# Optimization experiments

Hardware: AMD Instinct MI355X
Metric: run time of the kernel (lower is better)

Reference implementation:

```python
import jax, jax.numpy as jnp
import numpy as np

SEGMENT_LENGTHS = [2048, 4096, 8192]
DILATION_RATES = [1, 2, 4]
RING_SIZE = 4


def _head_groups(h, g):
    base, rem = divmod(h, g)
    return [base + (1 if i < rem else 0) for i in range(g)]


def _dilation_pattern(n, seg, r, group_idx):
    # Per-segment dilated index pattern of total length n (index_select target).
    s = min(seg, n)
    off = group_idx % r
    base = (off + np.arange(0, s, r)) % s          # stride-r indices within segment
    pat_seg = np.tile(base, r)[:s]                  # repeat to fill segment length
    nseg = n // s
    pat = (pat_seg[None, :] + np.arange(nseg)[:, None] * s).reshape(-1)
    return pat


def _apply_dilation(x):
    # x: (b, n, h, d). Gather along sequence per head group.
    b, n, h, d = x.shape
    groups = _head_groups(h, len(SEGMENT_LENGTHS))
    outs, hs = [], 0
    for i, (seg, r, g) in enumerate(zip(SEGMENT_LENGTHS, DILATION_RATES, groups)):
        if g == 0:
            continue
        pat = jnp.asarray(_dilation_pattern(n, seg, r, i))
        outs.append(x[:, pat, hs:hs + g, :])
        hs += g
    return jnp.concatenate(outs, axis=2)


def setup_inputs() -> dict:
    key = jax.random.key(0)
    k1, k2, k3 = jax.random.split(key, 3)
    shape = (1, 8192, 16, 64)
    return {
        "q": jax.random.normal(k1, shape, dtype=jnp.float32),
        "k": jax.random.normal(k2, shape, dtype=jnp.float32),
        "v": jax.random.normal(k3, shape, dtype=jnp.float32),
    }


def reference(q, k, v):
    b, n, h, d = q.shape
    scale = 1.0 / jnp.sqrt(jnp.asarray(d, q.dtype))
    chunk = n // RING_SIZE

    # Dilate queries once; dilate each local KV chunk (ring-distributed layout).
    qt = _apply_dilation(q).transpose(0, 2, 1, 3)   # (b, h, n, d)

    acc_out = jnp.zeros((b, h, n, d), q.dtype)
    acc_lse = jnp.full((b, h, n), -jnp.inf, q.dtype)

    # Simulated ring pass: iterate over KV chunks with online-LSE accumulation.
    for c in range(RING_SIZE):
        kc = _apply_dilation(k[:, c * chunk:(c + 1) * chunk])  # (b, chunk, h, d)
        vc = _apply_dilation(v[:, c * chunk:(c + 1) * chunk])
        scores = jnp.einsum('bhqd,bkhd->bhqk', qt, kc) * scale
        lse_c = jax.nn.logsumexp(scores, axis=-1)              # (b, h, n)
        out_c = jnp.einsum('bhqk,bkhd->bhqd',
                           jax.nn.softmax(scores, axis=-1), vc)
        new_lse = jnp.logaddexp(acc_lse, lse_c)
        w_old = jnp.exp(acc_lse - new_lse)[..., None]
        w_new = jnp.exp(lse_c - new_lse)[..., None]
        acc_out = w_old * acc_out + w_new * out_c
        acc_lse = new_lse

    return acc_out.transpose(0, 2, 1, 3)  # (b, n, h, d)
```

## Files before the change

kernel.cpp:

```cpp
#include <hip/hip_runtime.h>
#include <hip/hip_bf16.h>
#include <math.h>

typedef __attribute__((ext_vector_type(4))) float f32x4;
typedef __attribute__((ext_vector_type(8))) short bf16x8;
typedef __attribute__((ext_vector_type(4))) short s16x4;

#define NH 16
#define HD 64
#define BM 128
#define BN 64
#define WM 32
#define LDS_K 72
#define TILE_B 18432
#define TILE_S 9216
#define WS_NEEDED 23003136ull

#define OPART_OFF 23003136ull
#define LPART_OFF (OPART_OFF + 35651584ull)
#define WS2_NEEDED (LPART_OFF + 557056ull)

#define NSPLIT3 1856
#define OPART2_OFF 23003136ull
#define LPART2_OFF (OPART2_OFF + 60817408ull)
#define WS3_NEEDED (LPART2_OFF + 950272ull)

__device__ __forceinline__ short f2bf(float f) {
    union { float f; unsigned u; } x; x.f = f;
    unsigned r = x.u + 0x7fffu + ((x.u >> 16) & 1u);
    return (short)(r >> 16);
}
__device__ __forceinline__ unsigned pack2bf(float a, float b) {
    union { float f; unsigned u; } x, y; x.f = a; y.f = b;
    return __builtin_amdgcn_perm(y.u + 0x8000u, x.u + 0x8000u, 0x07060302u);
}
__device__ __forceinline__ float elem(const float4& r, int j) {
    return ((const float*)&r)[j];
}
__device__ __forceinline__ size_t head_base(int h) {
    if (h < 6)  return (size_t)h * (128 * TILE_B);
    if (h < 11) return 6ull * (128 * TILE_B) + (size_t)(h - 6) * (64 * TILE_B);
    return 6ull * (128 * TILE_B) + 5ull * (64 * TILE_B) + (size_t)(h - 11) * (32 * TILE_B);
}

__global__ __launch_bounds__(256)
void rda_pack(const float* __restrict__ K, const float* __restrict__ V, char* __restrict__ W) {
    int bid = blockIdx.x;
    int h, t, type;
    if (bid < 768)       { type = 0; h = bid >> 7;                t = bid & 127; }
    else if (bid < 1088) { type = 1; h = 6 + ((bid - 768) >> 6);  t = (bid - 768) & 63; }
    else                 { type = 2; h = 11 + ((bid - 1088) >> 5); t = (bid - 1088) & 31; }
    int rate = 1 << type, off = type;
    char* tile = W + head_base(h) + (size_t)t * TILE_B;
    int tid = threadIdx.x;
    {
        int row = tid >> 2, c = (tid & 3) * 16;
        int pos = rate * (t * 64 + row) + off;
        const float* p = K + ((size_t)pos * NH + h) * HD + c;
        float4 a0 = ((const float4*)p)[0], a1 = ((const float4*)p)[1];
        float4 a2 = ((const float4*)p)[2], a3 = ((const float4*)p)[3];
        uint4 d0, d1;
        d0.x = pack2bf(elem(a0,0), elem(a0,1)); d0.y = pack2bf(elem(a0,2), elem(a0,3));
        d0.z = pack2bf(elem(a1,0), elem(a1,1)); d0.w = pack2bf(elem(a1,2), elem(a1,3));
        d1.x = pack2bf(elem(a2,0), elem(a2,1)); d1.y = pack2bf(elem(a2,2), elem(a2,3));
        d1.z = pack2bf(elem(a3,0), elem(a3,1)); d1.w = pack2bf(elem(a3,2), elem(a3,3));
        char* dst = tile + row * (LDS_K * 2) + c * 2;
        ((uint4*)dst)[0] = d0;
        ((uint4*)dst)[1] = d1;
    }
    {
        int vr = (tid & 15) * 4, vc = (tid >> 4) * 4;
        float4 vv[4];
#pragma unroll
        for (int i = 0; i < 4; ++i) {
            int pos = rate * (t * 64 + vr + i) + off;
            vv[i] = *(const float4*)(V + ((size_t)pos * NH + h) * HD + vc);
        }
#pragma unroll
        for (int j = 0; j < 4; ++j) {
            uint2 w;
            w.x = pack2bf(elem(vv[0], j), elem(vv[1], j));
            w.y = pack2bf(elem(vv[2], j), elem(vv[3], j));
            *(uint2*)(tile + 9216 + (vc + j) * (LDS_K * 2) + vr * 2) = w;
        }
    }
}

__global__ __launch_bounds__(256, 3)
void rda_attn_ks2(const float* __restrict__ Q, char* __restrict__ W, float* __restrict__ O) {
    __shared__ __align__(16) short sKV[2 * TILE_S];
    __shared__ __align__(16) short sP[4][WM * 64];

    int bid = blockIdx.x;
    int h, mb, type, kc, sid;
    if (bid < 1536)      { type = 0; h = bid >> 8; int rem = bid & 255; mb = rem >> 2; kc = rem & 3; sid = bid; }
    else if (bid < 1856) { type = 1; int rel = bid - 1536; h = 6 + (rel >> 6); int rem = rel & 63; mb = rem >> 1; kc = rem & 1; sid = bid; }
    else                 { type = 2; int rel = bid - 1856; h = 11 + (rel >> 4); mb = rel & 15; kc = 0; sid = -1; }
    int rate = 1 << type;
    int off  = type;
    int kb0  = kc * 32;

    int tid  = threadIdx.x;
    int wave = tid >> 6;
    int lane = tid & 63;
    int ln   = lane & 15;
    int quad = lane >> 4;

    const float SC = 0.125f * 1.4426950408889634f;

    int qbase = mb * BM + wave * WM;
    bf16x8 qf[2][2];
#pragma unroll
    for (int mt = 0; mt < 2; ++mt) {
        int u = qbase + mt * 16 + ln;
        size_t base = ((size_t)(rate * u + off) * NH + h) * HD;
#pragma unroll
        for (int ks = 0; ks < 2; ++ks) {
            const float* p = Q + base + ks * 32 + quad * 8;
            float4 a = ((const float4*)p)[0];
            float4 b = ((const float4*)p)[1];
            union { uint4 u4; bf16x8 f; } cv;
            cv.u4.x = pack2bf(elem(a,0)*SC, elem(a,1)*SC);
            cv.u4.y = pack2bf(elem(a,2)*SC, elem(a,3)*SC);
            cv.u4.z = pack2bf(elem(b,0)*SC, elem(b,1)*SC);
            cv.u4.w = pack2bf(elem(b,2)*SC, elem(b,3)*SC);
            qf[mt][ks] = cv.f;
        }
    }

    f32x4 acc[2][4];
#pragma unroll
    for (int mt = 0; mt < 2; ++mt)
#pragma unroll
        for (int dt = 0; dt < 4; ++dt) acc[mt][dt] = (f32x4){0.f, 0.f, 0.f, 0.f};
    float lp[2] = {0.f, 0.f};

    const char* gh = W + head_base(h);

    auto stage = [&](const char* gt, int lB) {
#pragma unroll
        for (int r = 0; r < 4; ++r) {
            int c = r * 4096 + tid * 16;
            __builtin_amdgcn_global_load_lds(
                (const __attribute__((address_space(1))) unsigned*)(gt + c),
                (__attribute__((address_space(3))) unsigned*)((char*)sKV + lB + c),
                16, 0, 0);
        }
        if (tid < 128) {
            int c = 16384 + tid * 16;
            __builtin_amdgcn_global_load_lds(
                (const __attribute__((address_space(1))) unsigned*)(gt + c),
                (__attribute__((address_space(3))) unsigned*)((char*)sKV + lB + c),
                16, 0, 0);
        }
    };

    stage(gh + (size_t)kb0 * TILE_B, 0);
    int pB = 0;

    char* pbase = (char*)&sP[wave][0];

    for (int i = 0; i < 32; ++i) {
        int kb = kb0 + i;
        __syncthreads();

        if (i + 1 < 32) stage(gh + (size_t)(kb + 1) * TILE_B, pB ^ TILE_B);

        const short* sK  = (const short*)((const char*)sKV + pB);
        const short* sVT = sK + BN * LDS_K;

        f32x4 st[4][2];
        __builtin_amdgcn_s_setprio(1);
#pragma unroll
        for (int kt = 0; kt < 4; ++kt) {
            bf16x8 a0 = *(bf16x8*)&sK[(kt * 16 + ln) * LDS_K + quad * 8];
            bf16x8 a1 = *(bf16x8*)&sK[(kt * 16 + ln) * LDS_K + 32 + quad * 8];
#pragma unroll
            for (int mt = 0; mt < 2; ++mt) {
                f32x4 c = (f32x4){0.f, 0.f, 0.f, 0.f};
                c = __builtin_amdgcn_mfma_f32_16x16x32_bf16(a0, qf[mt][0], c, 0, 0, 0);
                c = __builtin_amdgcn_mfma_f32_16x16x32_bf16(a1, qf[mt][1], c, 0, 0, 0);
                st[kt][mt] = c;
            }
        }
        __builtin_amdgcn_s_setprio(0);

#pragma unroll
        for (int mt = 0; mt < 2; ++mt)
#pragma unroll
            for (int kt = 0; kt < 4; ++kt) {
                float p0 = __builtin_amdgcn_exp2f(st[kt][mt][0]);
                float p1 = __builtin_amdgcn_exp2f(st[kt][mt][1]);
                float p2 = __builtin_amdgcn_exp2f(st[kt][mt][2]);
                float p3 = __builtin_amdgcn_exp2f(st[kt][mt][3]);
                st[kt][mt][0] = p0; st[kt][mt][1] = p1;
                st[kt][mt][2] = p2; st[kt][mt][3] = p3;
                lp[mt] += (p0 + p1) + (p2 + p3);
            }

#pragma unroll
        for (int mt = 0; mt < 2; ++mt)
#pragma unroll
            for (int kt = 0; kt < 4; ++kt) {
                uint2 pk;
                pk.x = pack2bf(st[kt][mt][0], st[kt][mt][1]);
                pk.y = pack2bf(st[kt][mt][2], st[kt][mt][3]);
                int prow = mt * 16 + ln;
                int pbyte = (prow * 128 + (kt * 16 + quad * 4) * 2) ^ ((prow & 7) << 4);
                *(uint2*)(pbase + pbyte) = pk;
            }

        bf16x8 vbr[2][4];
#pragma unroll
        for (int ksk = 0; ksk < 2; ++ksk)
#pragma unroll
            for (int dt = 0; dt < 4; ++dt)
                vbr[ksk][dt] = *(bf16x8*)&sVT[(dt * 16 + ln) * LDS_K + ksk * 32 + quad * 8];

        __asm__ volatile("s_waitcnt lgkmcnt(0)" ::: "memory");

        __builtin_amdgcn_s_setprio(1);
#pragma unroll
        for (int ksk = 0; ksk < 2; ++ksk) {
            int b0 = (ln * 128 + (ksk * 32 + quad * 8) * 2) ^ ((ln & 7) << 4);
            int b1 = ((16 + ln) * 128 + (ksk * 32 + quad * 8) * 2) ^ ((ln & 7) << 4);
            bf16x8 pa0 = *(bf16x8*)(pbase + b0);
            bf16x8 pa1 = *(bf16x8*)(pbase + b1);
#pragma unroll
            for (int dt = 0; dt < 4; ++dt) {
                acc[0][dt] = __builtin_amdgcn_mfma_f32_16x16x32_bf16(pa0, vbr[ksk][dt], acc[0][dt], 0, 0, 0);
                acc[1][dt] = __builtin_amdgcn_mfma_f32_16x16x32_bf16(pa1, vbr[ksk][dt], acc[1][dt], 0, 0, 0);
            }
        }
        __builtin_amdgcn_s_setprio(0);
        pB ^= TILE_B;
    }

#pragma unroll
    for (int mt = 0; mt < 2; ++mt) {
        lp[mt] += __shfl_xor(lp[mt], 16);
        lp[mt] += __shfl_xor(lp[mt], 32);
    }

    if (type == 2) {
#pragma unroll
        for (int mt = 0; mt < 2; ++mt)
#pragma unroll
            for (int r = 0; r < 4; ++r) {
                float lO = __shfl(lp[mt], quad * 4 + r);
                float inv = 1.0f / lO;
                int u = qbase + mt * 16 + quad * 4 + r;
#pragma unroll
                for (int dt = 0; dt < 4; ++dt) {
                    float val = acc[mt][dt][r] * inv;
                    int dcol = dt * 16 + ln;
#pragma unroll
                    for (int t = 0; t < 4; ++t)
                        O[((size_t)(u + t * 2048) * NH + h) * HD + dcol] = val;
                }
            }
    } else {
        float* Op = (float*)(W + OPART2_OFF) + (size_t)sid * (BM * HD);
        float* Lp = (float*)(W + LPART2_OFF) + (size_t)sid * BM;
#pragma unroll
        for (int mt = 0; mt < 2; ++mt) {
            if (quad == 0) Lp[wave * WM + mt * 16 + ln] = lp[mt];
#pragma unroll
            for (int r = 0; r < 4; ++r) {
                int ql = wave * WM + mt * 16 + quad * 4 + r;
#pragma unroll
                for (int dt = 0; dt < 4; ++dt)
                    Op[ql * HD + dt * 16 + ln] = acc[mt][dt][r];
            }
        }
    }
}

__global__ __launch_bounds__(256)
void rda_comb2(const char* __restrict__ W, float* __restrict__ O) {
    int c = blockIdx.x;
    int h, mb, type, s0, np;
    if (c < 384) { type = 0; h = c >> 6;              mb = c & 63; s0 = (h * 64 + mb) * 4; np = 4; }
    else         { type = 1; int rel = c - 384; h = 6 + (rel >> 5); mb = rel & 31; s0 = 1536 + rel * 2; np = 2; }

    const float* P0 = (const float*)(W + OPART2_OFF) + (size_t)s0 * (BM * HD);
    const float* L0 = (const float*)(W + LPART2_OFF) + (size_t)s0 * BM;

    __shared__ float sInv[BM];
    int tid = threadIdx.x;
    if (tid < BM) {
        float s = L0[tid] + L0[BM + tid];
        if (np == 4) s += L0[2 * BM + tid] + L0[3 * BM + tid];
        sInv[tid] = 1.0f / s;
    }
    __syncthreads();

#pragma unroll
    for (int i = 0; i < 8; ++i) {
        int f = i * 256 + tid;
        int q = f >> 4, d4 = f & 15;
        float4 a = ((const float4*)P0)[f];
        float4 b = ((const float4*)(P0 + BM * HD))[f];
        float4 v;
        v.x = a.x + b.x; v.y = a.y + b.y; v.z = a.z + b.z; v.w = a.w + b.w;
        if (np == 4) {
            float4 e = ((const float4*)(P0 + 2 * BM * HD))[f];
            float4 g = ((const float4*)(P0 + 3 * BM * HD))[f];
            v.x += e.x + g.x; v.y += e.y + g.y; v.z += e.z + g.z; v.w += e.w + g.w;
        }
        float inv = sInv[q];
        v.x *= inv; v.y *= inv; v.z *= inv; v.w *= inv;
        int u = mb * BM + q;
        if (type == 0) {
            *(float4*)&O[((size_t)u * NH + h) * HD + d4 * 4] = v;
        } else {
            int r0 = ((u >> 11) << 12) + (u & 2047);
            *(float4*)&O[((size_t)r0 * NH + h) * HD + d4 * 4] = v;
            *(float4*)&O[((size_t)(r0 + 2048) * NH + h) * HD + d4 * 4] = v;
        }
    }
}

__global__ __launch_bounds__(256, 3)
void rda_attn_ks(const float* __restrict__ Q, char* __restrict__ W, float* __restrict__ O) {
    __shared__ __align__(16) short sKV[2 * TILE_S];
    __shared__ __align__(16) short sP[4][WM * 64];

    int bid = blockIdx.x;
    int h, mb, type, kc, nst, sid;
    if (bid < 768)       { type = 0; h = bid >> 7; int rem = bid & 127; mb = rem >> 1; kc = rem & 1; nst = 64; sid = bid; }
    else if (bid < 1088) { type = 1; int rel = bid - 768; h = 6 + (rel >> 6); int rem = rel & 63; mb = rem >> 1; kc = rem & 1; nst = 32; sid = bid; }
    else                 { type = 2; int rel = bid - 1088; h = 11 + (rel >> 4); mb = rel & 15; kc = 0; nst = 32; sid = -1; }
    int rate = 1 << type;
    int off  = type;
    int kb0  = kc * nst;

    int tid  = threadIdx.x;
    int wave = tid >> 6;
    int lane = tid & 63;
    int ln   = lane & 15;
    int quad = lane >> 4;

    const float SC = 0.125f * 1.4426950408889634f;

    int qbase = mb * BM + wave * WM;
    bf16x8 qf[2][2];
#pragma unroll
    for (int mt = 0; mt < 2; ++mt) {
        int u = qbase + mt * 16 + ln;
        size_t base = ((size_t)(rate * u + off) * NH + h) * HD;
#pragma unroll
        for (int ks = 0; ks < 2; ++ks) {
            const float* p = Q + base + ks * 32 + quad * 8;
            float4 a = ((const float4*)p)[0];
            float4 b = ((const float4*)p)[1];
            union { uint4 u4; bf16x8 f; } cv;
            cv.u4.x = pack2bf(elem(a,0)*SC, elem(a,1)*SC);
            cv.u4.y = pack2bf(elem(a,2)*SC, elem(a,3)*SC);
            cv.u4.z = pack2bf(elem(b,0)*SC, elem(b,1)*SC);
            cv.u4.w = pack2bf(elem(b,2)*SC, elem(b,3)*SC);
            qf[mt][ks] = cv.f;
        }
    }

    f32x4 acc[2][4];
#pragma unroll
    for (int mt = 0; mt < 2; ++mt)
#pragma unroll
        for (int dt = 0; dt < 4; ++dt) acc[mt][dt] = (f32x4){0.f, 0.f, 0.f, 0.f};
    float lp[2] = {0.f, 0.f};

    const char* gh = W + head_base(h);

    auto stage = [&](const char* gt, int lB) {
#pragma unroll
        for (int r = 0; r < 4; ++r) {
            int c = r * 4096 + tid * 16;
            __builtin_amdgcn_global_load_lds(
                (const __attribute__((address_space(1))) unsigned*)(gt + c),
                (__attribute__((address_space(3))) unsigned*)((char*)sKV + lB + c),
                16, 0, 0);
        }
        if (tid < 128) {
            int c = 16384 + tid * 16;
            __builtin_amdgcn_global_load_lds(
                (const __attribute__((address_space(1))) unsigned*)(gt + c),
                (__attribute__((address_space(3))) unsigned*)((char*)sKV + lB + c),
                16, 0, 0);
        }
    };

    stage(gh + (size_t)kb0 * TILE_B, 0);
    int pB = 0;
    char* pbase = (char*)&sP[wave][0];

    for (int i = 0; i < nst; ++i) {
        int kb = kb0 + i;
        __syncthreads();

        if (i + 1 < nst) stage(gh + (size_t)(kb + 1) * TILE_B, pB ^ TILE_B);

        const short* sK  = (const short*)((const char*)sKV + pB);
        const short* sVT = sK + BN * LDS_K;

        f32x4 st[4][2];
        __builtin_amdgcn_s_setprio(1);
#pragma unroll
        for (int kt = 0; kt < 4; ++kt) {
            bf16x8 a0 = *(bf16x8*)&sK[(kt * 16 + ln) * LDS_K + quad * 8];
            bf16x8 a1 = *(bf16x8*)&sK[(kt * 16 + ln) * LDS_K + 32 + quad * 8];
#pragma unroll
            for (int mt = 0; mt < 2; ++mt) {
                f32x4 c = (f32x4){0.f, 0.f, 0.f, 0.f};
                c = __builtin_amdgcn_mfma_f32_16x16x32_bf16(a0, qf[mt][0], c, 0, 0, 0);
                c = __builtin_amdgcn_mfma_f32_16x16x32_bf16(a1, qf[mt][1], c, 0, 0, 0);
                st[kt][mt] = c;
            }
        }
        __builtin_amdgcn_s_setprio(0);

#pragma unroll
        for (int mt = 0; mt < 2; ++mt)
#pragma unroll
            for (int kt = 0; kt < 4; ++kt) {
                float p0 = __builtin_amdgcn_exp2f(st[kt][mt][0]);
                float p1 = __builtin_amdgcn_exp2f(st[kt][mt][1]);
                float p2 = __builtin_amdgcn_exp2f(st[kt][mt][2]);
                float p3 = __builtin_amdgcn_exp2f(st[kt][mt][3]);
                st[kt][mt][0] = p0; st[kt][mt][1] = p1;
                st[kt][mt][2] = p2; st[kt][mt][3] = p3;
                lp[mt] += (p0 + p1) + (p2 + p3);
            }

#pragma unroll
        for (int mt = 0; mt < 2; ++mt)
#pragma unroll
            for (int kt = 0; kt < 4; ++kt) {
                uint2 pk;
                pk.x = pack2bf(st[kt][mt][0], st[kt][mt][1]);
                pk.y = pack2bf(st[kt][mt][2], st[kt][mt][3]);
                int prow = mt * 16 + ln;
                int pbyte = (prow * 128 + (kt * 16 + quad * 4) * 2) ^ ((prow & 7) << 4);
                *(uint2*)(pbase + pbyte) = pk;
            }
        __asm__ volatile("s_waitcnt lgkmcnt(0)" ::: "memory");

        __builtin_amdgcn_s_setprio(1);
#pragma unroll
        for (int ksk = 0; ksk < 2; ++ksk) {
            int b0 = (ln * 128 + (ksk * 32 + quad * 8) * 2) ^ ((ln & 7) << 4);
            int b1 = ((16 + ln) * 128 + (ksk * 32 + quad * 8) * 2) ^ ((ln & 7) << 4);
            bf16x8 pa0 = *(bf16x8*)(pbase + b0);
            bf16x8 pa1 = *(bf16x8*)(pbase + b1);
#pragma unroll
            for (int dt = 0; dt < 4; ++dt) {
                bf16x8 vb = *(bf16x8*)&sVT[(dt * 16 + ln) * LDS_K + ksk * 32 + quad * 8];
                acc[0][dt] = __builtin_amdgcn_mfma_f32_16x16x32_bf16(pa0, vb, acc[0][dt], 0, 0, 0);
                acc[1][dt] = __builtin_amdgcn_mfma_f32_16x16x32_bf16(pa1, vb, acc[1][dt], 0, 0, 0);
            }
        }
        __builtin_amdgcn_s_setprio(0);
        pB ^= TILE_B;
    }

#pragma unroll
    for (int mt = 0; mt < 2; ++mt) {
        lp[mt] += __shfl_xor(lp[mt], 16);
        lp[mt] += __shfl_xor(lp[mt], 32);
    }

    if (type == 2) {
#pragma unroll
        for (int mt = 0; mt < 2; ++mt)
#pragma unroll
            for (int r = 0; r < 4; ++r) {
                float lO = __shfl(lp[mt], quad * 4 + r);
                float inv = 1.0f / lO;
                int u = qbase + mt * 16 + quad * 4 + r;
#pragma unroll
                for (int dt = 0; dt < 4; ++dt) {
                    float val = acc[mt][dt][r] * inv;
                    int dcol = dt * 16 + ln;
#pragma unroll
                    for (int t = 0; t < 4; ++t)
                        O[((size_t)(u + t * 2048) * NH + h) * HD + dcol] = val;
                }
            }
    } else {
        float* Op = (float*)(W + OPART_OFF) + (size_t)sid * (BM * HD);
        float* Lp = (float*)(W + LPART_OFF) + (size_t)sid * BM;
#pragma unroll
        for (int mt = 0; mt < 2; ++mt) {
            if (quad == 0) Lp[wave * WM + mt * 16 + ln] = lp[mt];
#pragma unroll
            for (int r = 0; r < 4; ++r) {
                int ql = wave * WM + mt * 16 + quad * 4 + r;
#pragma unroll
                for (int dt = 0; dt < 4; ++dt)
                    Op[ql * HD + dt * 16 + ln] = acc[mt][dt][r];
            }
        }
    }
}

__global__ __launch_bounds__(256)
void rda_comb(const char* __restrict__ W, float* __restrict__ O) {
    int c = blockIdx.x;
    int h, mb, type, s0;
    if (c < 384) { type = 0; h = c >> 6;              mb = c & 63; s0 = c * 2; }
    else         { type = 1; int rel = c - 384; h = 6 + (rel >> 5); mb = rel & 31; s0 = 768 + rel * 2; }

    const float* P0 = (const float*)(W + OPART_OFF) + (size_t)s0 * (BM * HD);
    const float* P1 = P0 + BM * HD;
    const float* L0 = (const float*)(W + LPART_OFF) + (size_t)s0 * BM;
    const float* L1 = L0 + BM;

    __shared__ float sInv[BM];
    int tid = threadIdx.x;
    if (tid < BM) sInv[tid] = 1.0f / (L0[tid] + L1[tid]);
    __syncthreads();

#pragma unroll
    for (int i = 0; i < 8; ++i) {
        int f = i * 256 + tid;
        int q = f >> 4, d4 = f & 15;
        float4 a = ((const float4*)P0)[f];
        float4 b = ((const float4*)P1)[f];
        float inv = sInv[q];
        float4 v;
        v.x = (a.x + b.x) * inv; v.y = (a.y + b.y) * inv;
        v.z = (a.z + b.z) * inv; v.w = (a.w + b.w) * inv;
        int u = mb * BM + q;
        if (type == 0) {
            *(float4*)&O[((size_t)u * NH + h) * HD + d4 * 4] = v;
        } else {
            int r0 = ((u >> 11) << 12) + (u & 2047);
            *(float4*)&O[((size_t)r0 * NH + h) * HD + d4 * 4] = v;
            *(float4*)&O[((size_t)(r0 + 2048) * NH + h) * HD + d4 * 4] = v;
        }
    }
}

__global__ __launch_bounds__(256, 2)
void rda_attn_fb(const float* __restrict__ Q, const float* __restrict__ K,
                 const float* __restrict__ V, float* __restrict__ O) {
    __shared__ short sK[BN * LDS_K];
    __shared__ short sVT[HD * LDS_K];
    __shared__ short sP[4][WM * LDS_K];

    int bid = blockIdx.x;
    int h, mb, type;
    if (bid < 384)      { type = 0; h = bid >> 6;               mb = bid & 63; }
    else if (bid < 544) { type = 1; h = 6 + ((bid - 384) >> 5); mb = (bid - 384) & 31; }
    else                { type = 2; h = 11 + ((bid - 544) >> 4); mb = (bid - 544) & 15; }
    int rate = 1 << type;
    int off  = type;
    int nsteps = 128 >> type;

    int tid  = threadIdx.x;
    int wave = tid >> 6;
    int lane = tid & 63;
    int ln   = lane & 15;
    int quad = lane >> 4;

    const float SC = 0.125f * 1.4426950408889634f;

    int qbase = mb * BM + wave * WM;
    bf16x8 qf[2][2];
#pragma unroll
    for (int mt = 0; mt < 2; ++mt) {
        int u = qbase + mt * 16 + ln;
        size_t base = ((size_t)(rate * u + off) * NH + h) * HD;
#pragma unroll
        for (int ks = 0; ks < 2; ++ks) {
            const float* p = Q + base + ks * 32 + quad * 8;
            float4 a = ((const float4*)p)[0];
            float4 b = ((const float4*)p)[1];
            bf16x8 f;
#pragma unroll
            for (int i = 0; i < 4; ++i) { f[i] = f2bf(elem(a, i) * SC); f[4 + i] = f2bf(elem(b, i) * SC); }
            qf[mt][ks] = f;
        }
    }

    f32x4 acc[2][4];
#pragma unroll
    for (int mt = 0; mt < 2; ++mt)
#pragma unroll
        for (int dt = 0; dt < 4; ++dt) acc[mt][dt] = (f32x4){0.f, 0.f, 0.f, 0.f};
    float m_i[2] = {-INFINITY, -INFINITY};
    float l_i[2] = {0.f, 0.f};

    int srow = tid >> 2, sc0 = (tid & 3) * 16;
    int vr = (tid >> 4) * 4, vc = (tid & 15) * 4;

    for (int kb = 0; kb < nsteps; ++kb) {
        {
            int kpos = rate * (kb * BN + srow) + off;
            const float* p = K + ((size_t)kpos * NH + h) * HD + sc0;
            float4 kv0 = ((const float4*)p)[0], kv1 = ((const float4*)p)[1];
            float4 kv2 = ((const float4*)p)[2], kv3 = ((const float4*)p)[3];
            bf16x8 f0, f1;
#pragma unroll
            for (int i = 0; i < 4; ++i) {
                f0[i] = f2bf(elem(kv0, i)); f0[4 + i] = f2bf(elem(kv1, i));
                f1[i] = f2bf(elem(kv2, i)); f1[4 + i] = f2bf(elem(kv3, i));
            }
            *(bf16x8*)&sK[srow * LDS_K + sc0] = f0;
            *(bf16x8*)&sK[srow * LDS_K + sc0 + 8] = f1;
        }
        {
            float4 vv[4];
#pragma unroll
            for (int i = 0; i < 4; ++i) {
                int kpos = rate * (kb * BN + vr + i) + off;
                vv[i] = *(const float4*)(V + ((size_t)kpos * NH + h) * HD + vc);
            }
#pragma unroll
            for (int j = 0; j < 4; ++j) {
                s16x4 t;
                t[0] = f2bf(elem(vv[0], j)); t[1] = f2bf(elem(vv[1], j));
                t[2] = f2bf(elem(vv[2], j)); t[3] = f2bf(elem(vv[3], j));
                *(s16x4*)&sVT[(vc + j) * LDS_K + vr] = t;
            }
        }
        __syncthreads();

        f32x4 st[4][2];
#pragma unroll
        for (int kt = 0; kt < 4; ++kt) {
            bf16x8 a0 = *(bf16x8*)&sK[(kt * 16 + ln) * LDS_K + quad * 8];
            bf16x8 a1 = *(bf16x8*)&sK[(kt * 16 + ln) * LDS_K + 32 + quad * 8];
#pragma unroll
            for (int mt = 0; mt < 2; ++mt) {
                f32x4 c = (f32x4){0.f, 0.f, 0.f, 0.f};
                c = __builtin_amdgcn_mfma_f32_16x16x32_bf16(a0, qf[mt][0], c, 0, 0, 0);
                c = __builtin_amdgcn_mfma_f32_16x16x32_bf16(a1, qf[mt][1], c, 0, 0, 0);
                st[kt][mt] = c;
            }
        }

#pragma unroll
        for (int mt = 0; mt < 2; ++mt) {
            float tmax = -INFINITY;
#pragma unroll
            for (int kt = 0; kt < 4; ++kt)
#pragma unroll
                for (int r = 0; r < 4; ++r) tmax = fmaxf(tmax, st[kt][mt][r]);
            tmax = fmaxf(tmax, __shfl_xor(tmax, 16));
            tmax = fmaxf(tmax, __shfl_xor(tmax, 32));
            float mnew = fmaxf(m_i[mt], tmax);
            float al = exp2f(m_i[mt] - mnew);
            m_i[mt] = mnew;
            float rs = 0.f;
#pragma unroll
            for (int kt = 0; kt < 4; ++kt)
#pragma unroll
                for (int r = 0; r < 4; ++r) {
                    float pe = exp2f(st[kt][mt][r] - mnew);
                    st[kt][mt][r] = pe;
                    rs += pe;
                }
            rs += __shfl_xor(rs, 16);
            rs += __shfl_xor(rs, 32);
            l_i[mt] = l_i[mt] * al + rs;
#pragma unroll
            for (int r = 0; r < 4; ++r) {
                float aO = __shfl(al, quad * 4 + r);
#pragma unroll
                for (int dt = 0; dt < 4; ++dt) acc[mt][dt][r] *= aO;
            }
        }

#pragma unroll
        for (int mt = 0; mt < 2; ++mt)
#pragma unroll
            for (int kt = 0; kt < 4; ++kt) {
                s16x4 pk;
                pk[0] = f2bf(st[kt][mt][0]); pk[1] = f2bf(st[kt][mt][1]);
                pk[2] = f2bf(st[kt][mt][2]); pk[3] = f2bf(st[kt][mt][3]);
                *(s16x4*)&sP[wave][(mt * 16 + ln) * LDS_K + kt * 16 + quad * 4] = pk;
            }
        __asm__ volatile("s_waitcnt lgkmcnt(0)" ::: "memory");

#pragma unroll
        for (int ksk = 0; ksk < 2; ++ksk) {
            bf16x8 pa0 = *(bf16x8*)&sP[wave][(ln) * LDS_K + ksk * 32 + quad * 8];
            bf16x8 pa1 = *(bf16x8*)&sP[wave][(16 + ln) * LDS_K + ksk * 32 + quad * 8];
#pragma unroll
            for (int dt = 0; dt < 4; ++dt) {
                bf16x8 vb = *(bf16x8*)&sVT[(dt * 16 + ln) * LDS_K + ksk * 32 + quad * 8];
                acc[0][dt] = __builtin_amdgcn_mfma_f32_16x16x32_bf16(pa0, vb, acc[0][dt], 0, 0, 0);
                acc[1][dt] = __builtin_amdgcn_mfma_f32_16x16x32_bf16(pa1, vb, acc[1][dt], 0, 0, 0);
            }
        }
        __syncthreads();
    }

#pragma unroll
    for (int mt = 0; mt < 2; ++mt) {
#pragma unroll
        for (int r = 0; r < 4; ++r) {
            float lO = __shfl(l_i[mt], quad * 4 + r);
            float inv = 1.0f / lO;
            int u = qbase + mt * 16 + quad * 4 + r;
#pragma unroll
            for (int dt = 0; dt < 4; ++dt) {
                float val = acc[mt][dt][r] * inv;
                int dcol = dt * 16 + ln;
                if (type == 0) {
                    O[((size_t)u * NH + h) * HD + dcol] = val;
                } else if (type == 1) {
                    int r0 = ((u >> 11) << 12) + (u & 2047);
                    O[((size_t)r0 * NH + h) * HD + dcol] = val;
                    O[((size_t)(r0 + 2048) * NH + h) * HD + dcol] = val;
                } else {
#pragma unroll
                    for (int t = 0; t < 4; ++t)
                        O[((size_t)(u + t * 2048) * NH + h) * HD + dcol] = val;
                }
            }
        }
    }
}

extern "C" void kernel_launch(void* const* d_in, const int* in_sizes, int n_in,
                              void* d_out, int out_size, void* d_ws, size_t ws_size,
                              hipStream_t stream) {
    (void)in_sizes; (void)n_in; (void)out_size;
    const float* q = (const float*)d_in[0];
    const float* k = (const float*)d_in[1];
    const float* v = (const float*)d_in[2];
    float* o = (float*)d_out;
    if (ws_size >= WS3_NEEDED && d_ws != nullptr) {
        rda_pack<<<dim3(1248), dim3(256), 0, stream>>>(k, v, (char*)d_ws);
        rda_attn_ks2<<<dim3(1936), dim3(256), 0, stream>>>(q, (char*)d_ws, o);
        rda_comb2<<<dim3(544), dim3(256), 0, stream>>>((const char*)d_ws, o);
    } else if (ws_size >= WS2_NEEDED && d_ws != nullptr) {
        rda_pack<<<dim3(1248), dim3(256), 0, stream>>>(k, v, (char*)d_ws);
        rda_attn_ks<<<dim3(1168), dim3(256), 0, stream>>>(q, (char*)d_ws, o);
        rda_comb<<<dim3(544), dim3(256), 0, stream>>>((const char*)d_ws, o);
    } else {
        rda_attn_fb<<<dim3(624), dim3(256), 0, stream>>>(q, k, v, o);
    }
}
```

Measured before the change: 314.6 us.

## Use 8-wave 256-row query blocks so each staged KV tile is shared

Raises the attention kernel's query block from 128 to 256 rows by running 8 waves per 512-thread block, which halves the block count and the number of times each KV tile is staged into LDS. The combine kernel is resized to match, and V fragments are now read from LDS inside the MFMA loop instead of being preloaded, which lowers register pressure. The costs are fewer blocks to spread across CUs and possibly more LDS latency exposed in the PV loop.

```diff
diff --git a/kernel.cpp b/kernel.cpp
--- a/kernel.cpp
+++ b/kernel.cpp
@@ -9,6 +9,7 @@
 #define NH 16
 #define HD 64
 #define BM 128
+#define BM2 256
 #define BN 64
 #define WM 32
 #define LDS_K 72
@@ -20,7 +21,6 @@
 #define LPART_OFF (OPART_OFF + 35651584ull)
 #define WS2_NEEDED (LPART_OFF + 557056ull)
 
-#define NSPLIT3 1856
 #define OPART2_OFF 23003136ull
 #define LPART2_OFF (OPART2_OFF + 60817408ull)
 #define WS3_NEEDED (LPART2_OFF + 950272ull)
@@ -86,16 +86,16 @@
     }
 }
 
-__global__ __launch_bounds__(256, 3)
-void rda_attn_ks2(const float* __restrict__ Q, char* __restrict__ W, float* __restrict__ O) {
+__global__ __launch_bounds__(512, 4)
+void rda_attn_w8(const float* __restrict__ Q, char* __restrict__ W, float* __restrict__ O) {
     __shared__ __align__(16) short sKV[2 * TILE_S];
-    __shared__ __align__(16) short sP[4][WM * 64];
+    __shared__ __align__(16) short sP[8][WM * 64];
 
     int bid = blockIdx.x;
     int h, mb, type, kc, sid;
-    if (bid < 1536)      { type = 0; h = bid >> 8; int rem = bid & 255; mb = rem >> 2; kc = rem & 3; sid = bid; }
-    else if (bid < 1856) { type = 1; int rel = bid - 1536; h = 6 + (rel >> 6); int rem = rel & 63; mb = rem >> 1; kc = rem & 1; sid = bid; }
-    else                 { type = 2; int rel = bid - 1856; h = 11 + (rel >> 4); mb = rel & 15; kc = 0; sid = -1; }
+    if (bid < 768)      { type = 0; h = bid >> 7; int rem = bid & 127; mb = rem >> 2; kc = rem & 3; sid = bid; }
+    else if (bid < 928) { type = 1; int rel = bid - 768; h = 6 + (rel >> 5); int rem = rel & 31; mb = rem >> 1; kc = rem & 1; sid = bid; }
+    else                { type = 2; int rel = bid - 928; h = 11 + (rel >> 3); mb = rel & 7; kc = 0; sid = -1; }
     int rate = 1 << type;
     int off  = type;
     int kb0  = kc * 32;
@@ -108,7 +108,7 @@
 
     const float SC = 0.125f * 1.4426950408889634f;
 
-    int qbase = mb * BM + wave * WM;
+    int qbase = mb * BM2 + wave * WM;
     bf16x8 qf[2][2];
 #pragma unroll
     for (int mt = 0; mt < 2; ++mt) {
@@ -139,8 +139,8 @@
 
     auto stage = [&](const char* gt, int lB) {
 #pragma unroll
-        for (int r = 0; r < 4; ++r) {
-            int c = r * 4096 + tid * 16;
+        for (int r = 0; r < 2; ++r) {
+            int c = r * 8192 + tid * 16;
             __builtin_amdgcn_global_load_lds(
                 (const __attribute__((address_space(1))) unsigned*)(gt + c),
                 (__attribute__((address_space(3))) unsigned*)((char*)sKV + lB + c),
@@ -209,14 +209,6 @@
                 int pbyte = (prow * 128 + (kt * 16 + quad * 4) * 2) ^ ((prow & 7) << 4);
                 *(uint2*)(pbase + pbyte) = pk;
             }
-
-        bf16x8 vbr[2][4];
-#pragma unroll
-        for (int ksk = 0; ksk < 2; ++ksk)
-#pragma unroll
-            for (int dt = 0; dt < 4; ++dt)
-                vbr[ksk][dt] = *(bf16x8*)&sVT[(dt * 16 + ln) * LDS_K + ksk * 32 + quad * 8];
-
         __asm__ volatile("s_waitcnt lgkmcnt(0)" ::: "memory");
 
         __builtin_amdgcn_s_setprio(1);
@@ -228,8 +220,9 @@
             bf16x8 pa1 = *(bf16x8*)(pbase + b1);
 #pragma unroll
             for (int dt = 0; dt < 4; ++dt) {
-                acc[0][dt] = __builtin_amdgcn_mfma_f32_16x16x32_bf16(pa0, vbr[ksk][dt], acc[0][dt], 0, 0, 0);
-                acc[1][dt] = __builtin_amdgcn_mfma_f32_16x16x32_bf16(pa1, vbr[ksk][dt], acc[1][dt], 0, 0, 0);
+                bf16x8 vb = *(bf16x8*)&sVT[(dt * 16 + ln) * LDS_K + ksk * 32 + quad * 8];
+                acc[0][dt] = __builtin_amdgcn_mfma_f32_16x16x32_bf16(pa0, vb, acc[0][dt], 0, 0, 0);
+                acc[1][dt] = __builtin_amdgcn_mfma_f32_16x16x32_bf16(pa1, vb, acc[1][dt], 0, 0, 0);
             }
         }
         __builtin_amdgcn_s_setprio(0);
@@ -260,8 +253,8 @@
                 }
             }
     } else {
-        float* Op = (float*)(W + OPART2_OFF) + (size_t)sid * (BM * HD);
-        float* Lp = (float*)(W + LPART2_OFF) + (size_t)sid * BM;
+        float* Op = (float*)(W + OPART2_OFF) + (size_t)sid * (BM2 * HD);
+        float* Lp = (float*)(W + LPART2_OFF) + (size_t)sid * BM2;
 #pragma unroll
         for (int mt = 0; mt < 2; ++mt) {
             if (quad == 0) Lp[wave * WM + mt * 16 + ln] = lp[mt];
@@ -277,40 +270,40 @@
 }
 
 __global__ __launch_bounds__(256)
-void rda_comb2(const char* __restrict__ W, float* __restrict__ O) {
+void rda_comb3(const char* __restrict__ W, float* __restrict__ O) {
     int c = blockIdx.x;
     int h, mb, type, s0, np;
-    if (c < 384) { type = 0; h = c >> 6;              mb = c & 63; s0 = (h * 64 + mb) * 4; np = 4; }
-    else         { type = 1; int rel = c - 384; h = 6 + (rel >> 5); mb = rel & 31; s0 = 1536 + rel * 2; np = 2; }
-
-    const float* P0 = (const float*)(W + OPART2_OFF) + (size_t)s0 * (BM * HD);
-    const float* L0 = (const float*)(W + LPART2_OFF) + (size_t)s0 * BM;
-
-    __shared__ float sInv[BM];
+    if (c < 192) { type = 0; h = c >> 5;              mb = c & 31; s0 = (h * 32 + mb) * 4; np = 4; }
+    else         { type = 1; int rel = c - 192; h = 6 + (rel >> 4); mb = rel & 15; s0 = 768 + rel * 2; np = 2; }
+
+    const float* P0 = (const float*)(W + OPART2_OFF) + (size_t)s0 * (BM2 * HD);
+    const float* L0 = (const float*)(W + LPART2_OFF) + (size_t)s0 * BM2;
+
+    __shared__ float sInv[BM2];
     int tid = threadIdx.x;
-    if (tid < BM) {
-        float s = L0[tid] + L0[BM + tid];
-        if (np == 4) s += L0[2 * BM + tid] + L0[3 * BM + tid];
+    {
+        float s = L0[tid] + L0[BM2 + tid];
+        if (np == 4) s += L0[2 * BM2 + tid] + L0[3 * BM2 + tid];
         sInv[tid] = 1.0f / s;
     }
     __syncthreads();
 
 #pragma unroll
-    for (int i = 0; i < 8; ++i) {
+    for (int i = 0; i < 16; ++i) {
         int f = i * 256 + tid;
         int q = f >> 4, d4 = f & 15;
         float4 a = ((const float4*)P0)[f];
-        float4 b = ((const float4*)(P0 + BM * HD))[f];
+        float4 b = ((const float4*)(P0 + BM2 * HD))[f];
         float4 v;
         v.x = a.x + b.x; v.y = a.y + b.y; v.z = a.z + b.z; v.w = a.w + b.w;
         if (np == 4) {
-            float4 e = ((const float4*)(P0 + 2 * BM * HD))[f];
-            float4 g = ((const float4*)(P0 + 3 * BM * HD))[f];
+            float4 e = ((const float4*)(P0 + 2 * BM2 * HD))[f];
+            float4 g = ((const float4*)(P0 + 3 * BM2 * HD))[f];
             v.x += e.x + g.x; v.y += e.y + g.y; v.z += e.z + g.z; v.w += e.w + g.w;
         }
         float inv = sInv[q];
         v.x *= inv; v.y *= inv; v.z *= inv; v.w *= inv;
-        int u = mb * BM + q;
+        int u = mb * BM2 + q;
         if (type == 0) {
             *(float4*)&O[((size_t)u * NH + h) * HD + d4 * 4] = v;
         } else {
@@ -734,8 +727,8 @@
     float* o = (float*)d_out;
     if (ws_size >= WS3_NEEDED && d_ws != nullptr) {
         rda_pack<<<dim3(1248), dim3(256), 0, stream>>>(k, v, (char*)d_ws);
-        rda_attn_ks2<<<dim3(1936), dim3(256), 0, stream>>>(q, (char*)d_ws, o);
-        rda_comb2<<<dim3(544), dim3(256), 0, stream>>>((const char*)d_ws, o);
+        rda_attn_w8<<<dim3(968), dim3(512), 0, stream>>>(q, (char*)d_ws, o);
+        rda_comb3<<<dim3(272), dim3(256), 0, stream>>>((const char*)d_ws, o);
     } else if (ws_size >= WS2_NEEDED && d_ws != nullptr) {
         rda_pack<<<dim3(1248), dim3(256), 0, stream>>>(k, v, (char*)d_ws);
         rda_attn_ks<<<dim3(1168), dim3(256), 0, stream>>>(q, (char*)d_ws, o);
```

New measurement: 306.9 us. -2.4%, faster.
